# Optimization experiments

Measured on AMD Instinct MI355X. Metric: run time of the kernel, lower is better.

Reference implementation:

```python
import jax, jax.numpy as jnp
import numpy as np

E1, E2, A = 400000, 100000, 400000
F1, F2, FA, H = 128, 128, 8, 128


def _linear_init(key, fan_in, fan_out):
    # torch nn.Linear default: U(-1/sqrt(fan_in), 1/sqrt(fan_in)) for W and b
    kw, kb = jax.random.split(key)
    bound = 1.0 / np.sqrt(fan_in)
    W = jax.random.uniform(kw, (fan_in, fan_out), jnp.float32, -bound, bound)
    b = jax.random.uniform(kb, (fan_out,), jnp.float32, -bound, bound)
    return W, b


def setup_inputs() -> dict:
    key = jax.random.key(0)
    ks = jax.random.split(key, 10)
    e1 = jax.random.normal(ks[0], (E1, F1), jnp.float32)
    e2 = jax.random.normal(ks[1], (E2, F2), jnp.float32)
    a12 = jax.random.normal(ks[2], (A, FA), jnp.float32)
    row = jax.random.randint(ks[3], (A,), 0, E1)
    col = jax.random.randint(ks[4], (A,), 0, E2)
    angle_index12 = jnp.stack([row, col], axis=0)
    aW0, ab0 = _linear_init(ks[5], FA + F1 + F2, H)
    aW1, ab1 = _linear_init(ks[6], H, H)
    aW2, ab2 = _linear_init(ks[7], H, H)
    eW0, eb0 = _linear_init(ks[8], H + F2, H)
    k9a, k9b = jax.random.split(ks[9])
    eW1, eb1 = _linear_init(k9a, H, H)
    eW2, eb2 = _linear_init(k9b, H, H)
    return {"e1": e1, "e2": e2, "a12": a12, "angle_index12": angle_index12,
            "aW0": aW0, "ab0": ab0, "aW1": aW1, "ab1": ab1, "aW2": aW2, "ab2": ab2,
            "eW0": eW0, "eb0": eb0, "eW1": eW1, "eb1": eb1, "eW2": eW2, "eb2": eb2}


def _mlp(x, W0, b0, W1, b1, W2, b2):
    # linear -> SELU -> linear -> SELU -> linear (no final activation)
    h = jax.nn.selu(x @ W0 + b0)
    h = jax.nn.selu(h @ W1 + b1)
    return h @ W2 + b2


def reference(e1, e2, a12, angle_index12,
              aW0, ab0, aW1, ab1, aW2, ab2,
              eW0, eb0, eW1, eb1, eW2, eb2):
    row, col = angle_index12[0], angle_index12[1]
    # gather + concat: [A, FA+F1+F2]
    x = jnp.concatenate([a12, e1[row], e2[col]], axis=1)
    a = _mlp(x, aW0, ab0, aW1, ab1, aW2, ab2)  # [A, H]
    n2 = e2.shape[0]
    sums = jax.ops.segment_sum(a, col, num_segments=n2)  # [E2, H]
    cnt = jax.ops.segment_sum(jnp.ones((a.shape[0], 1), a.dtype), col, num_segments=n2)
    aggr = sums / jnp.maximum(cnt, 1.0)  # scatter-mean
    return _mlp(jnp.concatenate([aggr, e2], axis=1), eW0, eb0, eW1, eb1, eW2, eb2)
```

## Files before the change

### kernel.cpp

```cpp
#include <hip/hip_runtime.h>
#include <hip/hip_bf16.h>
#include <hip/hip_fp16.h>


using u16    = unsigned short;
using u16x8  = __attribute__((ext_vector_type(8))) unsigned short;
using bf16x8 = __attribute__((ext_vector_type(8))) short;
using f32x4  = __attribute__((ext_vector_type(4))) float;

constexpr int H   = 128;
constexpr int NTH = 256;

__device__ __forceinline__ u16 f2bf(float f) {
    union { float f; unsigned u; } x; x.f = f;
    unsigned r = x.u + 0x7FFFu + ((x.u >> 16) & 1u);
    return (u16)(r >> 16);
}
__device__ __forceinline__ unsigned cvt2(float x, float y) {
    union { __hip_bfloat162 h; unsigned u; } c;
    c.h = __float22bfloat162_rn(make_float2(x, y));
    return c.u;
}
__device__ __forceinline__ bf16x8 cvt8(float4 a, float4 b) {
    union { unsigned u[4]; bf16x8 v; } o;
    o.u[0] = cvt2(a.x, a.y); o.u[1] = cvt2(a.z, a.w);
    o.u[2] = cvt2(b.x, b.y); o.u[3] = cvt2(b.z, b.w);
    return o.v;
}
__device__ __forceinline__ float4 ld4(const float* p) { return *(const float4*)p; }
__device__ __forceinline__ float h2f(u16 u) {
    union { u16 u; __half h; } c; c.u = u;
    return __half2float(c.h);
}
__device__ __forceinline__ float selu_f(float x) {
    const float scale = 1.0507009873554804934193349852946f;
    const float sa    = 1.0507009873554805f * 1.6732632423543772848170429916717f;
    return x > 0.0f ? scale * x : sa * (__expf(x) - 1.0f);
}

__device__ __forceinline__ void load_wchunk(const u16* __restrict__ wt, int KPu, int c,
                                            int tid, u16x8 st[4]) {
#pragma unroll
    for (int s = 0; s < 4; ++s) {
        int i = s * NTH + tid;
        int n = i >> 3, jj = i & 7;
        st[s] = *(const u16x8*)(wt + (size_t)n * KPu + (c * 8 + jj) * 8);
    }
}
__device__ __forceinline__ void write_wchunk(u16* wb, int tid, const u16x8 st[4]) {
#pragma unroll
    for (int s = 0; s < 4; ++s) {
        int i = s * NTH + tid;
        *(u16x8*)(wb + i * 8) = st[s];
    }
}

template<int NKS>
__device__ __forceinline__ void mfma_chunk(const u16* cur, const bf16x8* afc,
                                           int ml, int kq, f32x4 acc[8]) {
#pragma unroll
    for (int ks = 0; ks < NKS; ++ks) {
        bf16x8 a = afc[ks];
#pragma unroll
        for (int sc = 0; sc < 8; ++sc) {
            bf16x8 b = *(const bf16x8*)&cur[(sc * 16 + ml) * 64 +
                                            (((ks * 4 + kq) ^ (ml & 7)) << 3)];
            acc[sc] = __builtin_amdgcn_mfma_f32_16x16x32_bf16(a, b, acc[sc], 0, 0, 0);
        }
    }
}

template<int NCHUNK, int LAST_NKS>
__device__ __forceinline__ void stream_layer(const u16* __restrict__ wt, int KPu,
                                             const bf16x8* af, u16* wb0, u16* wb1,
                                             int tid, int ml, int kq, f32x4 acc[8]) {
    u16x8 st[4];
    load_wchunk(wt, KPu, 0, tid, st);
    write_wchunk(wb0, tid, st);
    __syncthreads();
#pragma unroll
    for (int c = 0; c < NCHUNK; ++c) {
        u16* cur = (c & 1) ? wb1 : wb0;
        u16* nxt = (c & 1) ? wb0 : wb1;
        if (c + 1 < NCHUNK) load_wchunk(wt, KPu, c + 1, tid, st);
        if (c == NCHUNK - 1) mfma_chunk<LAST_NKS>(cur, af + 2 * c, ml, kq, acc);
        else                 mfma_chunk<2>(cur, af + 2 * c, ml, kq, acc);
        if (c + 1 < NCHUNK) write_wchunk(nxt, tid, st);
        __syncthreads();
    }
}

__device__ __forceinline__ void preload2_layer(const u16* __restrict__ wt,
                                               const bf16x8* af, u16* wb0, u16* wb1,
                                               int tid, int ml, int kq, f32x4 acc[8]) {
    u16x8 s0[4], s1[4];
    load_wchunk(wt, 128, 0, tid, s0);
    load_wchunk(wt, 128, 1, tid, s1);
    write_wchunk(wb0, tid, s0);
    write_wchunk(wb1, tid, s1);
    __syncthreads();
    mfma_chunk<2>(wb0, af + 0, ml, kq, acc);
    mfma_chunk<2>(wb1, af + 2, ml, kq, acc);
}

__device__ __forceinline__ void init_acc(const float* __restrict__ b, int ml, f32x4 acc[8]) {
#pragma unroll
    for (int sc = 0; sc < 8; ++sc) {
        float bv = b[sc * 16 + ml];
        acc[sc] = f32x4{bv, bv, bv, bv};
    }
}

__device__ __forceinline__ void store_h_selu(const f32x4 acc[8], u16* hbuf,
                                             int w, int ml, int kq) {
#pragma unroll
    for (int sc = 0; sc < 8; ++sc)
#pragma unroll
        for (int r = 0; r < 4; r += 2) {
            unsigned u = cvt2(selu_f(acc[sc][r]), selu_f(acc[sc][r + 1]));
            int rowb = w * 16 + kq * 4 + r;
            hbuf[rowb * 136 + sc * 16 + ml]       = (u16)u;
            hbuf[(rowb + 1) * 136 + sc * 16 + ml] = (u16)(u >> 16);
        }
}
__device__ __forceinline__ void read_af_h(const u16* hbuf, int w, int ml, int kq,
                                          bf16x8 af[4]) {
#pragma unroll
    for (int f = 0; f < 4; ++f)
        af[f] = *(const bf16x8*)&hbuf[(w * 16 + ml) * 136 + f * 32 + kq * 8];
}

__global__ void prep_weights(const float* __restrict__ aW0, const float* __restrict__ aW1,
                             const float* __restrict__ aW2, const float* __restrict__ eW0,
                             const float* __restrict__ eW1, const float* __restrict__ eW2,
                             u16* __restrict__ dst)
{
    int t = blockIdx.x * 256 + threadIdx.x;
    const int nbs[6]  = {40, 16, 16, 32, 16, 16};
    const int Ks[6]   = {264, 128, 128, 256, 128, 128};
    const int offs[6] = {0, 40960, 57344, 73728, 106496, 122880};
    const float* Ws[6] = {aW0, aW1, aW2, eW0, eW1, eW2};
    int m = 0, rem = t;
    for (m = 0; m < 6; ++m) { int c = 128 * nbs[m]; if (rem < c) break; rem -= c; }
    if (m >= 6) return;
    const int nb = nbs[m];
    const int n = rem / nb, j = rem % nb;
    const int c = j >> 3, jj = j & 7;
    const int kb = jj ^ (n & 7);
    const int k0 = c * 64 + kb * 8;
    const int K = Ks[m];
    const float* W = Ws[m];
    union { u16 u[8]; u16x8 v; } o;
#pragma unroll
    for (int i = 0; i < 8; ++i) {
        int k = k0 + i;
        o.u[i] = (k < K) ? f2bf(W[k * H + n]) : (u16)0;
    }
    *(u16x8*)&dst[offs[m] + n * (nb * 8) + j * 8] = o.v;
}

__global__ __launch_bounds__(NTH, 3) void angle_mlp(
    const float* __restrict__ e1, const float* __restrict__ e2,
    const float* __restrict__ a12, const int* __restrict__ idx,
    const u16* __restrict__ wt0, const u16* __restrict__ wt1, const u16* __restrict__ wt2,
    const float* __restrict__ b0, const float* __restrict__ b1, const float* __restrict__ b2,
    u16* __restrict__ sums, float* __restrict__ cnt, int A)
{
    __shared__ u16 wbuf[2][128 * 64];
    __shared__ u16 hbuf[64 * 136];

    const int tid = threadIdx.x;
    const int lane = tid & 63;
    const int ml = lane & 15, kq = lane >> 4;
    const int w = tid >> 6;
    const int ebase = blockIdx.x * 64;
    const int e = ebase + w * 16 + ml;
    const int rw = idx[e];
    const int cl = idx[A + e];
    if (kq == 0) atomicAdd(&cnt[cl], 1.0f);

    bf16x8 af[9];
    {
        const float* p1 = e1 + (size_t)rw * H;
        const float* p2 = e2 + (size_t)cl * H;
#pragma unroll
        for (int f = 0; f < 8; ++f) {
            int k0 = f * 32 + kq * 8;
            const float* p = (k0 == 0) ? (a12 + (size_t)e * 8)
                           : (k0 <= 128 ? p1 + (k0 - 8) : p2 + (k0 - 136));
            af[f] = cvt8(ld4(p), ld4(p + 4));
        }
        if (kq == 0) af[8] = cvt8(ld4(p2 + 120), ld4(p2 + 124));
        else { bf16x8 z = {0,0,0,0,0,0,0,0}; af[8] = z; }
    }

    f32x4 acc[8];
    init_acc(b0, ml, acc);
    stream_layer<5, 1>(wt0, 320, af, wbuf[0], wbuf[1], tid, ml, kq, acc);

    store_h_selu(acc, hbuf, w, ml, kq);
    __syncthreads();
    bf16x8 af1[4];
    read_af_h(hbuf, w, ml, kq, af1);
    init_acc(b1, ml, acc);
    preload2_layer(wt1, af1, wbuf[0], wbuf[1], tid, ml, kq, acc);

    __syncthreads();
    store_h_selu(acc, hbuf, w, ml, kq);
    __syncthreads();
    bf16x8 af2[4];
    read_af_h(hbuf, w, ml, kq, af2);
    init_acc(b2, ml, acc);
    preload2_layer(wt2, af2, wbuf[0], wbuf[1], tid, ml, kq, acc);

    const int rb = (ml & 1) * 2;
    const int i0 = A + ebase + w * 16 + kq * 4;
    const int clr0 = idx[i0 + rb];
    const int clr1 = idx[i0 + rb + 1];
#pragma unroll
    for (int sc = 0; sc < 8; ++sc) {
        float p0 = __shfl_xor(acc[sc][0], 1);
        float p1 = __shfl_xor(acc[sc][1], 1);
        float p2 = __shfl_xor(acc[sc][2], 1);
        float p3 = __shfl_xor(acc[sc][3], 1);
        float o0 = acc[sc][rb], o1 = acc[sc][rb + 1];
        float q0 = (ml & 1) ? p2 : p0;
        float q1 = (ml & 1) ? p3 : p1;
        float l0 = (ml & 1) ? q0 : o0, h0 = (ml & 1) ? o0 : q0;
        float l1 = (ml & 1) ? q1 : o1, h1 = (ml & 1) ? o1 : q1;
        union { __half2 h; unsigned u; } c0, c1;
        c0.h = __floats2half2_rn(l0, h0);
        c1.h = __floats2half2_rn(l1, h1);
        u16* d0 = sums + (size_t)clr0 * H + sc * 16 + (ml & ~1);
        u16* d1 = sums + (size_t)clr1 * H + sc * 16 + (ml & ~1);
        asm volatile("global_atomic_pk_add_f16 %0, %1, off" :: "v"(d0), "v"(c0.u) : "memory");
        asm volatile("global_atomic_pk_add_f16 %0, %1, off" :: "v"(d1), "v"(c1.u) : "memory");
    }
}

__global__ __launch_bounds__(NTH, 3) void edge_mlp(
    const float* __restrict__ e2, const u16* __restrict__ sums,
    const float* __restrict__ cnt,
    const u16* __restrict__ wt0, const u16* __restrict__ wt1, const u16* __restrict__ wt2,
    const float* __restrict__ b0, const float* __restrict__ b1, const float* __restrict__ b2,
    float* __restrict__ out, int E2n)
{
    __shared__ u16 wbuf[2][128 * 64];
    __shared__ u16 hbuf[64 * 136];

    const int tid = threadIdx.x;
    const int lane = tid & 63;
    const int ml = lane & 15, kq = lane >> 4;
    const int w = tid >> 6;
    const int nbase = blockIdx.x * 64;
    const int node = nbase + w * 16 + ml;
    const int nc = node < E2n ? node : E2n - 1;

    const float rcp = 1.0f / fmaxf(cnt[nc], 1.0f);
    bf16x8 af[8];
    {
        const u16* ps = sums + (size_t)nc * H;
        const float* p2 = e2 + (size_t)nc * H;
#pragma unroll
        for (int f = 0; f < 8; ++f) {
            int k0 = f * 32 + kq * 8;
            float4 lo, hi;
            if (k0 < 128) {
                u16x8 hv = *(const u16x8*)(ps + k0);
                lo.x = h2f(hv[0]) * rcp; lo.y = h2f(hv[1]) * rcp;
                lo.z = h2f(hv[2]) * rcp; lo.w = h2f(hv[3]) * rcp;
                hi.x = h2f(hv[4]) * rcp; hi.y = h2f(hv[5]) * rcp;
                hi.z = h2f(hv[6]) * rcp; hi.w = h2f(hv[7]) * rcp;
            } else {
                lo = ld4(p2 + (k0 - 128));
                hi = ld4(p2 + (k0 - 124));
            }
            af[f] = cvt8(lo, hi);
        }
    }

    f32x4 acc[8];
    init_acc(b0, ml, acc);
    stream_layer<4, 2>(wt0, 256, af, wbuf[0], wbuf[1], tid, ml, kq, acc);

    store_h_selu(acc, hbuf, w, ml, kq);
    __syncthreads();
    bf16x8 af1[4];
    read_af_h(hbuf, w, ml, kq, af1);
    init_acc(b1, ml, acc);
    preload2_layer(wt1, af1, wbuf[0], wbuf[1], tid, ml, kq, acc);

    __syncthreads();
    store_h_selu(acc, hbuf, w, ml, kq);
    __syncthreads();
    bf16x8 af2[4];
    read_af_h(hbuf, w, ml, kq, af2);
    init_acc(b2, ml, acc);
    preload2_layer(wt2, af2, wbuf[0], wbuf[1], tid, ml, kq, acc);

#pragma unroll
    for (int r = 0; r < 4; ++r) {
        int nrow = nbase + w * 16 + kq * 4 + r;
        if (nrow < E2n) {
            float* dst = out + (size_t)nrow * H + ml;
#pragma unroll
            for (int sc = 0; sc < 8; ++sc)
                dst[sc * 16] = acc[sc][r];
        }
    }
}

extern "C" void kernel_launch(void* const* d_in, const int* in_sizes, int n_in,
                              void* d_out, int out_size, void* d_ws, size_t ws_size,
                              hipStream_t stream)
{
    const float* e1  = (const float*)d_in[0];
    const float* e2  = (const float*)d_in[1];
    const float* a12 = (const float*)d_in[2];
    const int*   idx = (const int*)d_in[3];
    const float* aW0 = (const float*)d_in[4];
    const float* ab0 = (const float*)d_in[5];
    const float* aW1 = (const float*)d_in[6];
    const float* ab1 = (const float*)d_in[7];
    const float* aW2 = (const float*)d_in[8];
    const float* ab2 = (const float*)d_in[9];
    const float* eW0 = (const float*)d_in[10];
    const float* eb0 = (const float*)d_in[11];
    const float* eW1 = (const float*)d_in[12];
    const float* eb1 = (const float*)d_in[13];
    const float* eW2 = (const float*)d_in[14];
    const float* eb2 = (const float*)d_in[15];

    const int E2n = in_sizes[1] / H;
    const int A   = in_sizes[2] / 8;

    char* ws = (char*)d_ws;
    u16*   wdst   = (u16*)ws;
    u16*   sums_h = (u16*)(ws + 278528);
    float* cnt    = (float*)(ws + 278528 + (size_t)E2n * H * 2);

    hipMemsetAsync(sums_h, 0, (size_t)E2n * H * 2 + (size_t)E2n * 4, stream);
    prep_weights<<<dim3(68), dim3(256), 0, stream>>>(aW0, aW1, aW2, eW0, eW1, eW2, wdst);

    angle_mlp<<<dim3(A / 64), dim3(NTH), 0, stream>>>(
        e1, e2, a12, idx, wdst + 0, wdst + 40960, wdst + 57344,
        ab0, ab1, ab2, sums_h, cnt, A);

    edge_mlp<<<dim3((E2n + 63) / 64), dim3(NTH), 0, stream>>>(
        e2, sums_h, cnt, wdst + 73728, wdst + 106496, wdst + 122880,
        eb0, eb1, eb2, (float*)d_out, E2n);
}
```

Before: 295.7 us.

## Make angle MLP persistent with LDS-resident layer-0 weights and prefetched gathers

New measurement: 506.0 us. 71.1% more time.

```diff
diff --git a/kernel.cpp b/kernel.cpp
--- a/kernel.cpp
+++ b/kernel.cpp
@@ -159,82 +159,145 @@
     *(u16x8*)&dst[offs[m] + n * (nb * 8) + j * 8] = o.v;
 }
 
-__global__ __launch_bounds__(NTH, 3) void angle_mlp(
+__device__ __forceinline__ void issue_gather(float4 r[18],
+        const float* __restrict__ e1, const float* __restrict__ e2,
+        const float* __restrict__ a12, int e, int rw, int cl, int kq) {
+    const float* p1 = e1 + (size_t)rw * H;
+    const float* p2 = e2 + (size_t)cl * H;
+#pragma unroll
+    for (int f = 0; f < 8; ++f) {
+        int k0 = f * 32 + kq * 8;
+        const float* p = (k0 == 0) ? (a12 + (size_t)e * 8)
+                       : (k0 <= 128 ? p1 + (k0 - 8) : p2 + (k0 - 136));
+        r[2 * f]     = ld4(p);
+        r[2 * f + 1] = ld4(p + 4);
+    }
+    if (kq == 0) { r[16] = ld4(p2 + 120); r[17] = ld4(p2 + 124); }
+}
+__device__ __forceinline__ void conv_gather(const float4 r[18], bf16x8 af[9], int kq) {
+#pragma unroll
+    for (int f = 0; f < 8; ++f) af[f] = cvt8(r[2 * f], r[2 * f + 1]);
+    if (kq == 0) af[8] = cvt8(r[16], r[17]);
+    else { bf16x8 z = {0,0,0,0,0,0,0,0}; af[8] = z; }
+}
+
+__device__ __forceinline__ void layer0_lds(const u16* w0s, const bf16x8 af[9],
+                                           int ml, int kq, f32x4 acc[8]) {
+#pragma unroll
+    for (int ks = 0; ks < 9; ++ks) {
+        int B = ks * 4 + kq;
+        int off = ((B >> 3) * 8 + ((B & 7) ^ (ml & 7))) * 8;
+#pragma unroll
+        for (int sc = 0; sc < 8; ++sc) {
+            bf16x8 b = *(const bf16x8*)&w0s[(sc * 16 + ml) * 320 + off];
+            acc[sc] = __builtin_amdgcn_mfma_f32_16x16x32_bf16(af[ks], b, acc[sc], 0, 0, 0);
+        }
+    }
+}
+__device__ __forceinline__ void layer_gw(const u16* __restrict__ wt,
+                                         const bf16x8 afx[4], int ml, int kq,
+                                         f32x4 acc[8]) {
+#pragma unroll
+    for (int ks = 0; ks < 4; ++ks) {
+        int B = ks * 4 + kq;
+        int off = ((B >> 3) * 8 + ((B & 7) ^ (ml & 7))) * 8;
+#pragma unroll
+        for (int sc = 0; sc < 8; ++sc) {
+            bf16x8 b = *(const bf16x8*)&wt[(sc * 16 + ml) * 128 + off];
+            acc[sc] = __builtin_amdgcn_mfma_f32_16x16x32_bf16(afx[ks], b, acc[sc], 0, 0, 0);
+        }
+    }
+}
+
+__global__ __launch_bounds__(512, 2) void angle_mlp(
     const float* __restrict__ e1, const float* __restrict__ e2,
     const float* __restrict__ a12, const int* __restrict__ idx,
     const u16* __restrict__ wt0, const u16* __restrict__ wt1, const u16* __restrict__ wt2,
     const float* __restrict__ b0, const float* __restrict__ b1, const float* __restrict__ b2,
     u16* __restrict__ sums, float* __restrict__ cnt, int A)
 {
-    __shared__ u16 wbuf[2][128 * 64];
-    __shared__ u16 hbuf[64 * 136];
+    __shared__ u16 w0s[128 * 320];
+    __shared__ u16 hbuf[128 * 136];
 
     const int tid = threadIdx.x;
+#pragma unroll
+    for (int i = 0; i < 10; ++i) {
+        int j = i * 512 + tid;
+        *(u16x8*)&w0s[j * 8] = *(const u16x8*)&wt0[j * 8];
+    }
+    __syncthreads();
+
     const int lane = tid & 63;
     const int ml = lane & 15, kq = lane >> 4;
-    const int w = tid >> 6;
-    const int ebase = blockIdx.x * 64;
-    const int e = ebase + w * 16 + ml;
-    const int rw = idx[e];
-    const int cl = idx[A + e];
-    if (kq == 0) atomicAdd(&cnt[cl], 1.0f);
-
-    bf16x8 af[9];
-    {
-        const float* p1 = e1 + (size_t)rw * H;
-        const float* p2 = e2 + (size_t)cl * H;
-#pragma unroll
-        for (int f = 0; f < 8; ++f) {
-            int k0 = f * 32 + kq * 8;
-            const float* p = (k0 == 0) ? (a12 + (size_t)e * 8)
-                           : (k0 <= 128 ? p1 + (k0 - 8) : p2 + (k0 - 136));
-            af[f] = cvt8(ld4(p), ld4(p + 4));
-        }
-        if (kq == 0) af[8] = cvt8(ld4(p2 + 120), ld4(p2 + 124));
-        else { bf16x8 z = {0,0,0,0,0,0,0,0}; af[8] = z; }
-    }
-
-    f32x4 acc[8];
-    init_acc(b0, ml, acc);
-    stream_layer<5, 1>(wt0, 320, af, wbuf[0], wbuf[1], tid, ml, kq, acc);
-
-    store_h_selu(acc, hbuf, w, ml, kq);
-    __syncthreads();
-    bf16x8 af1[4];
-    read_af_h(hbuf, w, ml, kq, af1);
-    init_acc(b1, ml, acc);
-    preload2_layer(wt1, af1, wbuf[0], wbuf[1], tid, ml, kq, acc);
-
-    __syncthreads();
-    store_h_selu(acc, hbuf, w, ml, kq);
-    __syncthreads();
-    bf16x8 af2[4];
-    read_af_h(hbuf, w, ml, kq, af2);
-    init_acc(b2, ml, acc);
-    preload2_layer(wt2, af2, wbuf[0], wbuf[1], tid, ml, kq, acc);
-
-    const int rb = (ml & 1) * 2;
-    const int i0 = A + ebase + w * 16 + kq * 4;
-    const int clr0 = idx[i0 + rb];
-    const int clr1 = idx[i0 + rb + 1];
-#pragma unroll
-    for (int sc = 0; sc < 8; ++sc) {
-        float p0 = __shfl_xor(acc[sc][0], 1);
-        float p1 = __shfl_xor(acc[sc][1], 1);
-        float p2 = __shfl_xor(acc[sc][2], 1);
-        float p3 = __shfl_xor(acc[sc][3], 1);
-        float o0 = acc[sc][rb], o1 = acc[sc][rb + 1];
-        float q0 = (ml & 1) ? p2 : p0;
-        float q1 = (ml & 1) ? p3 : p1;
-        float l0 = (ml & 1) ? q0 : o0, h0 = (ml & 1) ? o0 : q0;
-        float l1 = (ml & 1) ? q1 : o1, h1 = (ml & 1) ? o1 : q1;
-        union { __half2 h; unsigned u; } c0, c1;
-        c0.h = __floats2half2_rn(l0, h0);
-        c1.h = __floats2half2_rn(l1, h1);
-        u16* d0 = sums + (size_t)clr0 * H + sc * 16 + (ml & ~1);
-        u16* d1 = sums + (size_t)clr1 * H + sc * 16 + (ml & ~1);
-        asm volatile("global_atomic_pk_add_f16 %0, %1, off" :: "v"(d0), "v"(c0.u) : "memory");
-        asm volatile("global_atomic_pk_add_f16 %0, %1, off" :: "v"(d1), "v"(c1.u) : "memory");
+    const int wv = tid >> 6;
+    u16* hb = hbuf + wv * (16 * 136);
+
+    const int NT = A >> 4;
+    int t = blockIdx.x * 8 + wv;
+
+    int e = t * 16 + ml;
+    int rw = idx[e];
+    int cl = idx[A + e];
+    float4 raw[18];
+    issue_gather(raw, e1, e2, a12, e, rw, cl, kq);
+
+    while (true) {
+        const int tn = t + 2048;
+        const bool last = tn >= NT;
+
+        bf16x8 af[9];
+        conv_gather(raw, af, kq);
+        if (kq == 0) atomicAdd(&cnt[cl], 1.0f);
+
+        int en = e, rwn = rw, cln = cl;
+        if (!last) { en = tn * 16 + ml; rwn = idx[en]; cln = idx[A + en]; }
+
+        f32x4 acc[8];
+        init_acc(b0, ml, acc);
+        layer0_lds(w0s, af, ml, kq, acc);
+
+        if (!last) issue_gather(raw, e1, e2, a12, en, rwn, cln, kq);
+
+        store_h_selu(acc, hb, 0, ml, kq);
+        bf16x8 af1[4];
+        read_af_h(hb, 0, ml, kq, af1);
+        init_acc(b1, ml, acc);
+        layer_gw(wt1, af1, ml, kq, acc);
+
+        store_h_selu(acc, hb, 0, ml, kq);
+        bf16x8 af2[4];
+        read_af_h(hb, 0, ml, kq, af2);
+        init_acc(b2, ml, acc);
+        layer_gw(wt2, af2, ml, kq, acc);
+
+        {
+            const int rb = (ml & 1) * 2;
+            const size_t i0 = (size_t)A + (size_t)t * 16 + kq * 4;
+            const int clr0 = idx[i0 + rb];
+            const int clr1 = idx[i0 + rb + 1];
+#pragma unroll
+            for (int sc = 0; sc < 8; ++sc) {
+                float p0 = __shfl_xor(acc[sc][0], 1);
+                float p1 = __shfl_xor(acc[sc][1], 1);
+                float p2 = __shfl_xor(acc[sc][2], 1);
+                float p3 = __shfl_xor(acc[sc][3], 1);
+                float o0 = acc[sc][rb], o1 = acc[sc][rb + 1];
+                float q0 = (ml & 1) ? p2 : p0;
+                float q1 = (ml & 1) ? p3 : p1;
+                float l0 = (ml & 1) ? q0 : o0, h0 = (ml & 1) ? o0 : q0;
+                float l1 = (ml & 1) ? q1 : o1, h1 = (ml & 1) ? o1 : q1;
+                union { __half2 h; unsigned u; } c0, c1;
+                c0.h = __floats2half2_rn(l0, h0);
+                c1.h = __floats2half2_rn(l1, h1);
+                u16* d0 = sums + (size_t)clr0 * H + sc * 16 + (ml & ~1);
+                u16* d1 = sums + (size_t)clr1 * H + sc * 16 + (ml & ~1);
+                asm volatile("global_atomic_pk_add_f16 %0, %1, off" :: "v"(d0), "v"(c0.u) : "memory");
+                asm volatile("global_atomic_pk_add_f16 %0, %1, off" :: "v"(d1), "v"(c1.u) : "memory");
+            }
+        }
+
+        if (last) break;
+        t = tn; e = en; rw = rwn; cl = cln;
     }
 }
 
@@ -342,7 +405,7 @@
     hipMemsetAsync(sums_h, 0, (size_t)E2n * H * 2 + (size_t)E2n * 4, stream);
     prep_weights<<<dim3(68), dim3(256), 0, stream>>>(aW0, aW1, aW2, eW0, eW1, eW2, wdst);
 
-    angle_mlp<<<dim3(A / 64), dim3(NTH), 0, stream>>>(
+    angle_mlp<<<dim3(256), dim3(512), 0, stream>>>(
         e1, e2, a12, idx, wdst + 0, wdst + 40960, wdst + 57344,
         ab0, ab1, ab2, sums_h, cnt, A);
 
```

## Swap MFMA operands so hidden activations stay in registers across angle MLP layers

Applied to the files above, without the earlier changes.

Result: slower. 444.9 us (+50.5%).

```diff
diff --git a/kernel.cpp b/kernel.cpp
--- a/kernel.cpp
+++ b/kernel.cpp
@@ -37,6 +37,18 @@
     const float sa    = 1.0507009873554805f * 1.6732632423543772848170429916717f;
     return x > 0.0f ? scale * x : sa * (__expf(x) - 1.0f);
 }
+__device__ __forceinline__ bf16x8 cvt8selu(f32x4 a, f32x4 b) {
+    union { unsigned u[4]; bf16x8 v; } o;
+    o.u[0] = cvt2(selu_f(a[0]), selu_f(a[1]));
+    o.u[1] = cvt2(selu_f(a[2]), selu_f(a[3]));
+    o.u[2] = cvt2(selu_f(b[0]), selu_f(b[1]));
+    o.u[3] = cvt2(selu_f(b[2]), selu_f(b[3]));
+    return o.v;
+}
+__device__ __forceinline__ int pperm(int p) {
+    int s = p >> 4, kq = (p >> 2) & 3, r = p & 3;
+    return 32 * (s & 3) + 8 * kq + 4 * (s >> 2) + r;
+}
 
 __device__ __forceinline__ void load_wchunk(const u16* __restrict__ wt, int KPu, int c,
                                             int tid, u16x8 st[4]) {
@@ -64,6 +76,20 @@
 #pragma unroll
         for (int sc = 0; sc < 8; ++sc) {
             bf16x8 b = *(const bf16x8*)&cur[(sc * 16 + ml) * 64 +
+                                            (((ks * 4 + kq) ^ (ml & 7)) << 3)];
+            acc[sc] = __builtin_amdgcn_mfma_f32_16x16x32_bf16(a, b, acc[sc], 0, 0, 0);
+        }
+    }
+}
+template<int NKS>
+__device__ __forceinline__ void mfma_chunk_sw(const u16* cur, const bf16x8* bfc,
+                                              int ml, int kq, f32x4 acc[8]) {
+#pragma unroll
+    for (int ks = 0; ks < NKS; ++ks) {
+        bf16x8 b = bfc[ks];
+#pragma unroll
+        for (int sc = 0; sc < 8; ++sc) {
+            bf16x8 a = *(const bf16x8*)&cur[(sc * 16 + ml) * 64 +
                                             (((ks * 4 + kq) ^ (ml & 7)) << 3)];
             acc[sc] = __builtin_amdgcn_mfma_f32_16x16x32_bf16(a, b, acc[sc], 0, 0, 0);
         }
@@ -89,6 +115,25 @@
         __syncthreads();
     }
 }
+template<int NCHUNK, int LAST_NKS>
+__device__ __forceinline__ void stream_layer_sw(const u16* __restrict__ wt, int KPu,
+                                                const bf16x8* bf, u16* wb0, u16* wb1,
+                                                int tid, int ml, int kq, f32x4 acc[8]) {
+    u16x8 st[4];
+    load_wchunk(wt, KPu, 0, tid, st);
+    write_wchunk(wb0, tid, st);
+    __syncthreads();
+#pragma unroll
+    for (int c = 0; c < NCHUNK; ++c) {
+        u16* cur = (c & 1) ? wb1 : wb0;
+        u16* nxt = (c & 1) ? wb0 : wb1;
+        if (c + 1 < NCHUNK) load_wchunk(wt, KPu, c + 1, tid, st);
+        if (c == NCHUNK - 1) mfma_chunk_sw<LAST_NKS>(cur, bf + 2 * c, ml, kq, acc);
+        else                 mfma_chunk_sw<2>(cur, bf + 2 * c, ml, kq, acc);
+        if (c + 1 < NCHUNK) write_wchunk(nxt, tid, st);
+        __syncthreads();
+    }
+}
 
 __device__ __forceinline__ void preload2_layer(const u16* __restrict__ wt,
                                                const bf16x8* af, u16* wb0, u16* wb1,
@@ -102,6 +147,18 @@
     mfma_chunk<2>(wb0, af + 0, ml, kq, acc);
     mfma_chunk<2>(wb1, af + 2, ml, kq, acc);
 }
+__device__ __forceinline__ void preload2_layer_sw(const u16* __restrict__ wt,
+                                                  const bf16x8* bf, u16* wb0, u16* wb1,
+                                                  int tid, int ml, int kq, f32x4 acc[8]) {
+    u16x8 s0[4], s1[4];
+    load_wchunk(wt, 128, 0, tid, s0);
+    load_wchunk(wt, 128, 1, tid, s1);
+    write_wchunk(wb0, tid, s0);
+    write_wchunk(wb1, tid, s1);
+    __syncthreads();
+    mfma_chunk_sw<2>(wb0, bf + 0, ml, kq, acc);
+    mfma_chunk_sw<2>(wb1, bf + 2, ml, kq, acc);
+}
 
 __device__ __forceinline__ void init_acc(const float* __restrict__ b, int ml, f32x4 acc[8]) {
 #pragma unroll
@@ -130,12 +187,18 @@
         af[f] = *(const bf16x8*)&hbuf[(w * 16 + ml) * 136 + f * 32 + kq * 8];
 }
 
-__global__ void prep_weights(const float* __restrict__ aW0, const float* __restrict__ aW1,
+__global__ void prep_weights(const float* __restrict__ aW0, const float* __restrict__ ab0,
+                             const float* __restrict__ aW1, const float* __restrict__ ab1,
                              const float* __restrict__ aW2, const float* __restrict__ eW0,
                              const float* __restrict__ eW1, const float* __restrict__ eW2,
-                             u16* __restrict__ dst)
+                             u16* __restrict__ dst, float* __restrict__ b1p)
 {
     int t = blockIdx.x * 256 + threadIdx.x;
+    if (t >= 17408) {
+        int i = t - 17408;
+        if (i < 128) b1p[i] = ab1[pperm(i)];
+        return;
+    }
     const int nbs[6]  = {40, 16, 16, 32, 16, 16};
     const int Ks[6]   = {264, 128, 128, 256, 128, 128};
     const int offs[6] = {0, 40960, 57344, 73728, 106496, 122880};
@@ -150,24 +213,45 @@
     const int k0 = c * 64 + kb * 8;
     const int K = Ks[m];
     const float* W = Ws[m];
+    const int nc = (m <= 1) ? pperm(n) : n;
     union { u16 u[8]; u16x8 v; } o;
 #pragma unroll
     for (int i = 0; i < 8; ++i) {
         int k = k0 + i;
-        o.u[i] = (k < K) ? f2bf(W[k * H + n]) : (u16)0;
+        float fv;
+        if (m == 0)      fv = (k < 264) ? aW0[k * H + nc] : (k == 264 ? ab0[nc] : 0.0f);
+        else if (m == 1) fv = (k < 128) ? aW1[k * H + nc] : 0.0f;
+        else             fv = (k < K) ? W[k * H + n] : 0.0f;
+        o.u[i] = f2bf(fv);
     }
     *(u16x8*)&dst[offs[m] + n * (nb * 8) + j * 8] = o.v;
 }
 
-__global__ __launch_bounds__(NTH, 3) void angle_mlp(
+__device__ __forceinline__ void gather_af(bf16x8 af[9],
+        const float* __restrict__ e1, const float* __restrict__ e2,
+        const float* __restrict__ a12, int e, int rw, int cl, int kq) {
+    const float* p1 = e1 + (size_t)rw * H;
+    const float* p2 = e2 + (size_t)cl * H;
+#pragma unroll
+    for (int f = 0; f < 8; ++f) {
+        int k0 = f * 32 + kq * 8;
+        const float* p = (k0 == 0) ? (a12 + (size_t)e * 8)
+                       : (k0 <= 128 ? p1 + (k0 - 8) : p2 + (k0 - 136));
+        af[f] = cvt8(ld4(p), ld4(p + 4));
+    }
+    if (kq == 0)      af[8] = cvt8(ld4(p2 + 120), ld4(p2 + 124));
+    else if (kq == 1) { bf16x8 o = {(short)0x3F80, 0, 0, 0, 0, 0, 0, 0}; af[8] = o; }
+    else              { bf16x8 z = {0, 0, 0, 0, 0, 0, 0, 0}; af[8] = z; }
+}
+
+__global__ __launch_bounds__(NTH, 5) void angle_mlp(
     const float* __restrict__ e1, const float* __restrict__ e2,
     const float* __restrict__ a12, const int* __restrict__ idx,
     const u16* __restrict__ wt0, const u16* __restrict__ wt1, const u16* __restrict__ wt2,
-    const float* __restrict__ b0, const float* __restrict__ b1, const float* __restrict__ b2,
+    const float* __restrict__ b1p, const float* __restrict__ b2g,
     u16* __restrict__ sums, float* __restrict__ cnt, int A)
 {
     __shared__ u16 wbuf[2][128 * 64];
-    __shared__ u16 hbuf[64 * 136];
 
     const int tid = threadIdx.x;
     const int lane = tid & 63;
@@ -180,62 +264,34 @@
     if (kq == 0) atomicAdd(&cnt[cl], 1.0f);
 
     bf16x8 af[9];
-    {
-        const float* p1 = e1 + (size_t)rw * H;
-        const float* p2 = e2 + (size_t)cl * H;
-#pragma unroll
-        for (int f = 0; f < 8; ++f) {
-            int k0 = f * 32 + kq * 8;
-            const float* p = (k0 == 0) ? (a12 + (size_t)e * 8)
-                           : (k0 <= 128 ? p1 + (k0 - 8) : p2 + (k0 - 136));
-            af[f] = cvt8(ld4(p), ld4(p + 4));
-        }
-        if (kq == 0) af[8] = cvt8(ld4(p2 + 120), ld4(p2 + 124));
-        else { bf16x8 z = {0,0,0,0,0,0,0,0}; af[8] = z; }
-    }
+    gather_af(af, e1, e2, a12, e, rw, cl, kq);
 
     f32x4 acc[8];
-    init_acc(b0, ml, acc);
-    stream_layer<5, 1>(wt0, 320, af, wbuf[0], wbuf[1], tid, ml, kq, acc);
-
-    store_h_selu(acc, hbuf, w, ml, kq);
-    __syncthreads();
-    bf16x8 af1[4];
-    read_af_h(hbuf, w, ml, kq, af1);
-    init_acc(b1, ml, acc);
-    preload2_layer(wt1, af1, wbuf[0], wbuf[1], tid, ml, kq, acc);
-
-    __syncthreads();
-    store_h_selu(acc, hbuf, w, ml, kq);
-    __syncthreads();
-    bf16x8 af2[4];
-    read_af_h(hbuf, w, ml, kq, af2);
-    init_acc(b2, ml, acc);
-    preload2_layer(wt2, af2, wbuf[0], wbuf[1], tid, ml, kq, acc);
-
-    const int rb = (ml & 1) * 2;
-    const int i0 = A + ebase + w * 16 + kq * 4;
-    const int clr0 = idx[i0 + rb];
-    const int clr1 = idx[i0 + rb + 1];
-#pragma unroll
-    for (int sc = 0; sc < 8; ++sc) {
-        float p0 = __shfl_xor(acc[sc][0], 1);
-        float p1 = __shfl_xor(acc[sc][1], 1);
-        float p2 = __shfl_xor(acc[sc][2], 1);
-        float p3 = __shfl_xor(acc[sc][3], 1);
-        float o0 = acc[sc][rb], o1 = acc[sc][rb + 1];
-        float q0 = (ml & 1) ? p2 : p0;
-        float q1 = (ml & 1) ? p3 : p1;
-        float l0 = (ml & 1) ? q0 : o0, h0 = (ml & 1) ? o0 : q0;
-        float l1 = (ml & 1) ? q1 : o1, h1 = (ml & 1) ? o1 : q1;
-        union { __half2 h; unsigned u; } c0, c1;
-        c0.h = __floats2half2_rn(l0, h0);
-        c1.h = __floats2half2_rn(l1, h1);
-        u16* d0 = sums + (size_t)clr0 * H + sc * 16 + (ml & ~1);
-        u16* d1 = sums + (size_t)clr1 * H + sc * 16 + (ml & ~1);
-        asm volatile("global_atomic_pk_add_f16 %0, %1, off" :: "v"(d0), "v"(c0.u) : "memory");
-        asm volatile("global_atomic_pk_add_f16 %0, %1, off" :: "v"(d1), "v"(c1.u) : "memory");
-    }
+#pragma unroll
+    for (int sc = 0; sc < 8; ++sc) acc[sc] = f32x4{0.f, 0.f, 0.f, 0.f};
+    stream_layer_sw<5, 1>(wt0, 320, af, wbuf[0], wbuf[1], tid, ml, kq, acc);
+
+    bf16x8 hq[4];
+#pragma unroll
+    for (int ks = 0; ks < 4; ++ks) hq[ks] = cvt8selu(acc[ks], acc[ks + 4]);
+#pragma unroll
+    for (int sc = 0; sc < 8; ++sc) acc[sc] = *(const f32x4*)&b1p[sc * 16 + kq * 4];
+    preload2_layer_sw(wt1, hq, wbuf[0], wbuf[1], tid, ml, kq, acc);
+
+#pragma unroll
+    for (int ks = 0; ks < 4; ++ks) hq[ks] = cvt8selu(acc[ks], acc[ks + 4]);
+#pragma unroll
+    for (int sc = 0; sc < 8; ++sc) acc[sc] = *(const f32x4*)&b2g[sc * 16 + kq * 4];
+    __syncthreads();
+    preload2_layer_sw(wt2, hq, wbuf[0], wbuf[1], tid, ml, kq, acc);
+
+    __half2* dst = (__half2*)(sums + (size_t)cl * H + kq * 4);
+#pragma unroll
+    for (int sc = 0; sc < 8; ++sc)
+#pragma unroll
+        for (int q = 0; q < 2; ++q)
+            unsafeAtomicAdd(dst + sc * 8 + q,
+                            __floats2half2_rn(acc[sc][2 * q], acc[sc][2 * q + 1]));
 }
 
 __global__ __launch_bounds__(NTH, 3) void edge_mlp(
@@ -338,13 +394,15 @@
     u16*   wdst   = (u16*)ws;
     u16*   sums_h = (u16*)(ws + 278528);
     float* cnt    = (float*)(ws + 278528 + (size_t)E2n * H * 2);
+    float* b1p    = (float*)(ws + 278528 + (size_t)E2n * H * 2 + (size_t)E2n * 4);
 
     hipMemsetAsync(sums_h, 0, (size_t)E2n * H * 2 + (size_t)E2n * 4, stream);
-    prep_weights<<<dim3(68), dim3(256), 0, stream>>>(aW0, aW1, aW2, eW0, eW1, eW2, wdst);
+    prep_weights<<<dim3(69), dim3(256), 0, stream>>>(
+        aW0, ab0, aW1, ab1, aW2, eW0, eW1, eW2, wdst, b1p);
 
     angle_mlp<<<dim3(A / 64), dim3(NTH), 0, stream>>>(
         e1, e2, a12, idx, wdst + 0, wdst + 40960, wdst + 57344,
-        ab0, ab1, ab2, sums_h, cnt, A);
+        b1p, ab2, sums_h, cnt, A);
 
     edge_mlp<<<dim3((E2n + 63) / 64), dim3(NTH), 0, stream>>>(
         e2, sums_h, cnt, wdst + 73728, wdst + 106496, wdst + 122880,
```

## Process two 64-angle tiles per block, prefetching second tile's gathers during first

Applied to the files above, without the earlier changes.

New measurement: 313.2 us. 5.9% more time.

```diff
diff --git a/kernel.cpp b/kernel.cpp
--- a/kernel.cpp
+++ b/kernel.cpp
@@ -159,51 +159,23 @@
     *(u16x8*)&dst[offs[m] + n * (nb * 8) + j * 8] = o.v;
 }
 
-__global__ __launch_bounds__(NTH, 3) void angle_mlp(
-    const float* __restrict__ e1, const float* __restrict__ e2,
-    const float* __restrict__ a12, const int* __restrict__ idx,
-    const u16* __restrict__ wt0, const u16* __restrict__ wt1, const u16* __restrict__ wt2,
-    const float* __restrict__ b0, const float* __restrict__ b1, const float* __restrict__ b2,
-    u16* __restrict__ sums, float* __restrict__ cnt, int A)
-{
-    __shared__ u16 wbuf[2][128 * 64];
-    __shared__ u16 hbuf[64 * 136];
-
-    const int tid = threadIdx.x;
-    const int lane = tid & 63;
-    const int ml = lane & 15, kq = lane >> 4;
-    const int w = tid >> 6;
-    const int ebase = blockIdx.x * 64;
-    const int e = ebase + w * 16 + ml;
-    const int rw = idx[e];
-    const int cl = idx[A + e];
-    if (kq == 0) atomicAdd(&cnt[cl], 1.0f);
-
-    bf16x8 af[9];
-    {
-        const float* p1 = e1 + (size_t)rw * H;
-        const float* p2 = e2 + (size_t)cl * H;
-#pragma unroll
-        for (int f = 0; f < 8; ++f) {
-            int k0 = f * 32 + kq * 8;
-            const float* p = (k0 == 0) ? (a12 + (size_t)e * 8)
-                           : (k0 <= 128 ? p1 + (k0 - 8) : p2 + (k0 - 136));
-            af[f] = cvt8(ld4(p), ld4(p + 4));
-        }
-        if (kq == 0) af[8] = cvt8(ld4(p2 + 120), ld4(p2 + 124));
-        else { bf16x8 z = {0,0,0,0,0,0,0,0}; af[8] = z; }
-    }
-
-    f32x4 acc[8];
+__device__ __forceinline__ void angle_pass(const bf16x8 af[9],
+        const u16* __restrict__ wt0, const u16* __restrict__ wt1,
+        const u16* __restrict__ wt2,
+        const float* __restrict__ b0, const float* __restrict__ b1,
+        const float* __restrict__ b2,
+        u16* wbuf0, u16* wbuf1, u16* hbuf,
+        int tid, int w, int ml, int kq, f32x4 acc[8])
+{
     init_acc(b0, ml, acc);
-    stream_layer<5, 1>(wt0, 320, af, wbuf[0], wbuf[1], tid, ml, kq, acc);
+    stream_layer<5, 1>(wt0, 320, af, wbuf0, wbuf1, tid, ml, kq, acc);
 
     store_h_selu(acc, hbuf, w, ml, kq);
     __syncthreads();
     bf16x8 af1[4];
     read_af_h(hbuf, w, ml, kq, af1);
     init_acc(b1, ml, acc);
-    preload2_layer(wt1, af1, wbuf[0], wbuf[1], tid, ml, kq, acc);
+    preload2_layer(wt1, af1, wbuf0, wbuf1, tid, ml, kq, acc);
 
     __syncthreads();
     store_h_selu(acc, hbuf, w, ml, kq);
@@ -211,8 +183,13 @@
     bf16x8 af2[4];
     read_af_h(hbuf, w, ml, kq, af2);
     init_acc(b2, ml, acc);
-    preload2_layer(wt2, af2, wbuf[0], wbuf[1], tid, ml, kq, acc);
-
+    preload2_layer(wt2, af2, wbuf0, wbuf1, tid, ml, kq, acc);
+}
+
+__device__ __forceinline__ void scatter_pass(const f32x4 acc[8],
+        const int* __restrict__ idx, u16* __restrict__ sums,
+        int A, int ebase, int w, int ml, int kq)
+{
     const int rb = (ml & 1) * 2;
     const int i0 = A + ebase + w * 16 + kq * 4;
     const int clr0 = idx[i0 + rb];
@@ -238,6 +215,103 @@
     }
 }
 
+__global__ __launch_bounds__(NTH, 3) void angle_mlp(
+    const float* __restrict__ e1, const float* __restrict__ e2,
+    const float* __restrict__ a12, const int* __restrict__ idx,
+    const u16* __restrict__ wt0, const u16* __restrict__ wt1, const u16* __restrict__ wt2,
+    const float* __restrict__ b0, const float* __restrict__ b1, const float* __restrict__ b2,
+    u16* __restrict__ sums, float* __restrict__ cnt, int A)
+{
+    __shared__ u16 wbuf[2][128 * 64];
+    __shared__ u16 hbuf[64 * 136];
+
+    const int tid = threadIdx.x;
+    const int lane = tid & 63;
+    const int ml = lane & 15, kq = lane >> 4;
+    const int w = tid >> 6;
+    const int ebase = blockIdx.x * 128;
+    const int ea = ebase + w * 16 + ml;
+    const int eb = ea + 64;
+    const int rwa = idx[ea], cla = idx[A + ea];
+    const int rwb = idx[eb], clb = idx[A + eb];
+    if (kq == 0) { atomicAdd(&cnt[cla], 1.0f); atomicAdd(&cnt[clb], 1.0f); }
+
+    bf16x8 af[9];
+    {
+        const float* p1 = e1 + (size_t)rwa * H;
+        const float* p2 = e2 + (size_t)cla * H;
+#pragma unroll
+        for (int f = 0; f < 8; ++f) {
+            int k0 = f * 32 + kq * 8;
+            const float* p = (k0 == 0) ? (a12 + (size_t)ea * 8)
+                           : (k0 <= 128 ? p1 + (k0 - 8) : p2 + (k0 - 136));
+            af[f] = cvt8(ld4(p), ld4(p + 4));
+        }
+        if (kq == 0) af[8] = cvt8(ld4(p2 + 120), ld4(p2 + 124));
+        else { bf16x8 z = {0,0,0,0,0,0,0,0}; af[8] = z; }
+    }
+
+    float4 raw1[16];
+    {
+        const float* p1 = e1 + (size_t)rwb * H;
+#pragma unroll
+        for (int f = 0; f < 4; ++f) {
+            int k0 = f * 32 + kq * 8;
+            const float* p = (k0 == 0) ? (a12 + (size_t)eb * 8) : (p1 + (k0 - 8));
+            raw1[2 * f]     = ld4(p);
+            raw1[2 * f + 1] = ld4(p + 4);
+        }
+    }
+
+    f32x4 acc[8];
+    init_acc(b0, ml, acc);
+    stream_layer<5, 1>(wt0, 320, af, wbuf[0], wbuf[1], tid, ml, kq, acc);
+
+    {
+        const float* p1 = e1 + (size_t)rwb * H;
+        const float* p2 = e2 + (size_t)clb * H;
+#pragma unroll
+        for (int f = 4; f < 8; ++f) {
+            int k0 = f * 32 + kq * 8;
+            const float* p = (k0 <= 128) ? (p1 + (k0 - 8)) : (p2 + (k0 - 136));
+            raw1[2 * f]     = ld4(p);
+            raw1[2 * f + 1] = ld4(p + 4);
+        }
+    }
+
+    store_h_selu(acc, hbuf, w, ml, kq);
+    __syncthreads();
+    {
+        bf16x8 af1[4];
+        read_af_h(hbuf, w, ml, kq, af1);
+        init_acc(b1, ml, acc);
+        preload2_layer(wt1, af1, wbuf[0], wbuf[1], tid, ml, kq, acc);
+    }
+    __syncthreads();
+    store_h_selu(acc, hbuf, w, ml, kq);
+    __syncthreads();
+    {
+        bf16x8 af2[4];
+        read_af_h(hbuf, w, ml, kq, af2);
+        init_acc(b2, ml, acc);
+        preload2_layer(wt2, af2, wbuf[0], wbuf[1], tid, ml, kq, acc);
+    }
+    scatter_pass(acc, idx, sums, A, ebase, w, ml, kq);
+
+    __syncthreads();
+
+    {
+        const float* p2 = e2 + (size_t)clb * H;
+#pragma unroll
+        for (int f = 0; f < 8; ++f) af[f] = cvt8(raw1[2 * f], raw1[2 * f + 1]);
+        if (kq == 0) af[8] = cvt8(ld4(p2 + 120), ld4(p2 + 124));
+        else { bf16x8 z = {0,0,0,0,0,0,0,0}; af[8] = z; }
+    }
+    angle_pass(af, wt0, wt1, wt2, b0, b1, b2,
+               wbuf[0], wbuf[1], hbuf, tid, w, ml, kq, acc);
+    scatter_pass(acc, idx, sums, A, ebase + 64, w, ml, kq);
+}
+
 __global__ __launch_bounds__(NTH, 3) void edge_mlp(
     const float* __restrict__ e2, const u16* __restrict__ sums,
     const float* __restrict__ cnt,
@@ -342,7 +416,7 @@
     hipMemsetAsync(sums_h, 0, (size_t)E2n * H * 2 + (size_t)E2n * 4, stream);
     prep_weights<<<dim3(68), dim3(256), 0, stream>>>(aW0, aW1, aW2, eW0, eW1, eW2, wdst);
 
-    angle_mlp<<<dim3(A / 64), dim3(NTH), 0, stream>>>(
+    angle_mlp<<<dim3(A / 128), dim3(NTH), 0, stream>>>(
         e1, e2, a12, idx, wdst + 0, wdst + 40960, wdst + 57344,
         ab0, ab1, ab2, sums_h, cnt, A);
 
```
